# Performance work log

Hardware: AMD Instinct MI355X
Metric: run time of the kernel (lower is better)

Reference implementation:

```python
import jax, jax.numpy as jnp
import numpy as np

V, E, HD, K = 100000, 128, 256, 9
B, T = 128, 512
H = HD // 2  # per-direction hidden size


def setup_inputs() -> dict:
    key = jax.random.key(0)
    ks = jax.random.split(key, 16)
    s = 0.1
    rn = lambda k, shape: jax.random.normal(k, shape, jnp.float32) * s
    sentences = jax.random.randint(ks[0], (B, T), 0, V, dtype=jnp.int32)
    lengths = jax.random.randint(ks[1], (B,), 1, T + 1, dtype=jnp.int32)
    return {
        'sentences': sentences,
        'lengths': lengths,
        'embed': rn(ks[2], (V, E)),
        'Wih_f': rn(ks[3], (4 * H, E)), 'Whh_f': rn(ks[4], (4 * H, H)),
        'bih_f': rn(ks[5], (4 * H,)), 'bhh_f': rn(ks[6], (4 * H,)),
        'Wih_b': rn(ks[7], (4 * H, E)), 'Whh_b': rn(ks[8], (4 * H, H)),
        'bih_b': rn(ks[9], (4 * H,)), 'bhh_b': rn(ks[10], (4 * H,)),
        'W_out': rn(ks[11], (K, HD)), 'b_out': rn(ks[12], (K,)),
        'start_t': rn(ks[13], (K,)), 'end_t': rn(ks[14], (K,)),
        'trans': rn(ks[15], (K, K)),
    }


def _lstm(x, mask, Wih, Whh, bih, bhh, reverse):
    # x: [B,T,E], mask: [B,T] bool. Replicates packed-sequence semantics:
    # state frozen and output zeroed at padding positions (padding is trailing,
    # so reverse=True starts fresh at each sequence's true end).
    Bv, Hv = x.shape[0], Whh.shape[1]
    bias = bih + bhh

    def step(carry, inp):
        h, c = carry
        x_t, m_t = inp  # [B,E], [B,1]
        gates = x_t @ Wih.T + h @ Whh.T + bias  # [B,4H]
        i, f, g, o = jnp.split(gates, 4, axis=-1)  # torch gate order i,f,g,o
        c_new = jax.nn.sigmoid(f) * c + jax.nn.sigmoid(i) * jnp.tanh(g)
        h_new = jax.nn.sigmoid(o) * jnp.tanh(c_new)
        h = jnp.where(m_t, h_new, h)
        c = jnp.where(m_t, c_new, c)
        return (h, c), h * m_t.astype(h.dtype)

    init = (jnp.zeros((Bv, Hv), x.dtype), jnp.zeros((Bv, Hv), x.dtype))
    xs = (jnp.swapaxes(x, 0, 1), jnp.swapaxes(mask, 0, 1)[..., None])
    _, hs = jax.lax.scan(step, init, xs, reverse=reverse)
    return jnp.swapaxes(hs, 0, 1)  # [B,T,H]


def _emissions(sentences, mask, embed, Wih_f, Whh_f, bih_f, bhh_f,
               Wih_b, Whh_b, bih_b, bhh_b, W_out, b_out):
    x = embed[sentences]  # [B,T,E] (dropout is identity at inference)
    hf = _lstm(x, mask, Wih_f, Whh_f, bih_f, bhh_f, reverse=False)
    hb = _lstm(x, mask, Wih_b, Whh_b, bih_b, bhh_b, reverse=True)
    h = jnp.concatenate([hf, hb], axis=-1)  # [B,T,2H]
    return jnp.einsum('btd,kd->btk', h, W_out) + b_out  # [B,T,K]


def _viterbi(em, mask, start_t, end_t, trans):
    # torchcrf-style batched Viterbi decode. em: [B,T,K], mask: [B,T] bool.
    Kv = em.shape[-1]
    ident = jnp.arange(Kv, dtype=jnp.int32)[None]  # identity backpointers for pads
    score0 = start_t[None] + em[:, 0]  # [B,K]

    def step(score, inp):
        em_t, m_t = inp  # [B,K], [B,1]
        cand = score[:, :, None] + trans[None] + em_t[:, None, :]  # [B,K_prev,K_cur]
        new_score = cand.max(axis=1)
        idx = cand.argmax(axis=1).astype(jnp.int32)  # [B,K]
        score = jnp.where(m_t, new_score, score)
        idx = jnp.where(m_t, idx, ident)
        return score, idx

    xs = (jnp.swapaxes(em[:, 1:], 0, 1), jnp.swapaxes(mask[:, 1:], 0, 1)[..., None])
    score, hist = jax.lax.scan(step, score0, xs)  # hist: [T-1,B,K]
    score = score + end_t[None]
    last_tag = jnp.argmax(score, axis=-1).astype(jnp.int32)  # [B]

    def back(tag, idx_t):
        prev = jnp.take_along_axis(idx_t, tag[:, None], axis=1)[:, 0]
        return prev, prev

    _, tags_prev = jax.lax.scan(back, last_tag, hist, reverse=True)  # [T-1,B]
    tags = jnp.swapaxes(jnp.concatenate([tags_prev, last_tag[None]], axis=0), 0, 1)
    return jnp.where(mask, tags, 0), score.max(axis=-1)


def reference(sentences, lengths, embed, Wih_f, Whh_f, bih_f, bhh_f,
              Wih_b, Whh_b, bih_b, bhh_b, W_out, b_out, start_t, end_t, trans):
    mask = jnp.arange(sentences.shape[1])[None] < lengths[:, None]  # [B,T]
    em = _emissions(sentences, mask, embed, Wih_f, Whh_f, bih_f, bhh_f,
                    Wih_b, Whh_b, bih_b, bhh_b, W_out, b_out)
    tags, _ = _viterbi(em, mask, start_t, end_t, trans)
    return tags  # [B,T] int32, padded positions set to 0
```

## Files before the change

kernel.cpp:

```cpp
#include <hip/hip_runtime.h>
#include <cmath>

#define B_  128
#define T_  512
#define E_  128
#define H_  128
#define G4  512
#define K_  9

__global__ __launch_bounds__(256, 2)
void proj_gemm(const int* __restrict__ sent, const float* __restrict__ embed,
               const float* __restrict__ Wf, const float* __restrict__ Wb,
               const float* __restrict__ bif, const float* __restrict__ bhf,
               const float* __restrict__ bib, const float* __restrict__ bhb,
               float* __restrict__ proj, int t0f, int Tc)
{
  __shared__ __align__(16) float Al[128 * 64];
  __shared__ __align__(16) float Bl[128 * 64];
  const int tid   = threadIdx.x;
  const int ntile = blockIdx.x;
  const int mtile = blockIdx.y;
  const int tpb   = Tc >> 6;
  const int b     = mtile / tpb;
  const int toff  = (mtile - b * tpb) << 6;
  const int dir   = ntile >> 3;
  const int t0    = dir ? (T_ - t0f - Tc) : t0f;
  const float* __restrict__ W = dir ? Wb : Wf;
  const int n0 = (ntile & 7) << 6;

  {
    const int r  = tid & 63;
    const int kc = tid >> 6;
    const int t  = t0 + toff + r;
    const int vid = sent[b * T_ + t];
    const float* arow = embed + (size_t)vid * E_ + kc * 32;
    const float* brow = W + (size_t)(n0 + r) * E_ + kc * 32;
#pragma unroll
    for (int q = 0; q < 8; ++q) {
      float4 av = *(const float4*)(arow + q * 4);
      float4 bv = *(const float4*)(brow + q * 4);
      int k0 = kc * 32 + q * 4;
      Al[(k0 + 0) * 64 + r] = av.x; Al[(k0 + 1) * 64 + r] = av.y;
      Al[(k0 + 2) * 64 + r] = av.z; Al[(k0 + 3) * 64 + r] = av.w;
      Bl[(k0 + 0) * 64 + r] = bv.x; Bl[(k0 + 1) * 64 + r] = bv.y;
      Bl[(k0 + 2) * 64 + r] = bv.z; Bl[(k0 + 3) * 64 + r] = bv.w;
    }
  }
  __syncthreads();

  const int mg = tid & 15, ng = tid >> 4;
  float acc[4][4] = {};
#pragma unroll 8
  for (int k = 0; k < 128; ++k) {
    float4 a  = *(const float4*)&Al[k * 64 + mg * 4];
    float4 bb = *(const float4*)&Bl[k * 64 + ng * 4];
    acc[0][0] += a.x * bb.x; acc[0][1] += a.x * bb.y; acc[0][2] += a.x * bb.z; acc[0][3] += a.x * bb.w;
    acc[1][0] += a.y * bb.x; acc[1][1] += a.y * bb.y; acc[1][2] += a.y * bb.z; acc[1][3] += a.y * bb.w;
    acc[2][0] += a.z * bb.x; acc[2][1] += a.z * bb.y; acc[2][2] += a.z * bb.z; acc[2][3] += a.z * bb.w;
    acc[3][0] += a.w * bb.x; acc[3][1] += a.w * bb.y; acc[3][2] += a.w * bb.z; acc[3][3] += a.w * bb.w;
  }

  const float* bi = dir ? bib : bif;
  const float* bh = dir ? bhb : bhf;
  const int nl = ng * 4;
  float4 bias;
  bias.x = bi[n0 + nl + 0] + bh[n0 + nl + 0];
  bias.y = bi[n0 + nl + 1] + bh[n0 + nl + 1];
  bias.z = bi[n0 + nl + 2] + bh[n0 + nl + 2];
  bias.w = bi[n0 + nl + 3] + bh[n0 + nl + 3];
#pragma unroll
  for (int i = 0; i < 4; ++i) {
    const int tloc = toff + mg * 4 + i;
    float4 o;
    o.x = acc[i][0] + bias.x; o.y = acc[i][1] + bias.y;
    o.z = acc[i][2] + bias.z; o.w = acc[i][3] + bias.w;
    *(float4*)&proj[((size_t)(b * Tc + tloc)) * 1024 + dir * G4 + n0 + nl] = o;
  }
}

__global__ __launch_bounds__(512, 2)
void lstm_chunk(const float* __restrict__ proj,
                const float* __restrict__ Whf, const float* __restrict__ Whb,
                const int* __restrict__ lengths,
                float* __restrict__ hs,
                float* __restrict__ sh, float* __restrict__ sc,
                int t0f, int Tc, int first)
{
  const int dir = blockIdx.x;
  const int b   = blockIdx.y;
  const int tid = threadIdx.x;
  const float* __restrict__ Whh = dir ? Whb : Whf;
  __shared__ __align__(16) float h_lds[H_];
  __shared__ float gates[G4];

  float w[128];
  {
    const float* wr = Whh + (size_t)tid * H_;
#pragma unroll
    for (int k = 0; k < 128; k += 4) {
      float4 v = *(const float4*)(wr + k);
      w[k] = v.x; w[k + 1] = v.y; w[k + 2] = v.z; w[k + 3] = v.w;
    }
  }
  const int len = lengths[b];
  const int t0  = dir ? (T_ - t0f - Tc) : t0f;
  float c = 0.f;
  if (tid < H_) {
    if (first) {
      h_lds[tid] = 0.f;
    } else {
      h_lds[tid] = sh[(dir * B_ + b) * H_ + tid];
      c          = sc[(dir * B_ + b) * H_ + tid];
    }
  }
  __syncthreads();

  const float* projp = proj + (size_t)b * Tc * 1024 + dir * G4 + tid;
  for (int s = 0; s < Tc; ++s) {
    const int tc = dir ? (Tc - 1 - s) : s;
    const int t  = t0 + tc;
    float acc = projp[(size_t)tc * 1024];
#pragma unroll
    for (int k4 = 0; k4 < 32; ++k4) {
      float4 h4 = *(const float4*)&h_lds[k4 * 4];
      acc += w[4 * k4 + 0] * h4.x; acc += w[4 * k4 + 1] * h4.y;
      acc += w[4 * k4 + 2] * h4.z; acc += w[4 * k4 + 3] * h4.w;
    }
    const int blk = tid >> 7;
    gates[tid] = (blk == 2) ? tanhf(acc) : 1.f / (1.f + expf(-acc));
    __syncthreads();
    if (tid < H_) {
      float gi = gates[tid], gf = gates[tid + 128];
      float gg = gates[tid + 256], go = gates[tid + 384];
      float cn = gf * c + gi * gg;
      float hn = go * tanhf(cn);
      bool  m  = (t < len);
      float hold = h_lds[tid];
      c = m ? cn : c;
      h_lds[tid] = m ? hn : hold;
      hs[(size_t)(b * T_ + t) * 256 + dir * H_ + tid] = m ? hn : 0.f;
    }
    __syncthreads();
  }
  if (tid < H_) {
    sh[(dir * B_ + b) * H_ + tid] = h_lds[tid];
    sc[(dir * B_ + b) * H_ + tid] = c;
  }
}

__global__ __launch_bounds__(256)
void emis_kernel(const float* __restrict__ hs, const float* __restrict__ Wout,
                 const float* __restrict__ bout, float* __restrict__ em)
{
  __shared__ __align__(16) float Wl[K_ * 256];
  const int tid = threadIdx.x;
  for (int i = tid; i < K_ * 256; i += 256) Wl[i] = Wout[i];
  __syncthreads();
  const int m = blockIdx.x * 256 + tid;
  const float* h = hs + (size_t)m * 256;
  float acc[K_] = {};
#pragma unroll 4
  for (int kk = 0; kk < 64; ++kk) {
    float4 h4 = *(const float4*)(h + kk * 4);
#pragma unroll
    for (int k9 = 0; k9 < K_; ++k9) {
      float4 w4 = *(const float4*)&Wl[k9 * 256 + kk * 4];
      acc[k9] += h4.x * w4.x + h4.y * w4.y + h4.z * w4.z + h4.w * w4.w;
    }
  }
#pragma unroll
  for (int k9 = 0; k9 < K_; ++k9) em[(size_t)m * K_ + k9] = acc[k9] + bout[k9];
}

__global__ __launch_bounds__(64)
void viterbi_kernel(const float* __restrict__ em, const int* __restrict__ lengths,
                    const float* __restrict__ st, const float* __restrict__ en,
                    const float* __restrict__ trans, int* __restrict__ tags)
{
  const int b    = blockIdx.x;
  const int lane = threadIdx.x;
  __shared__ unsigned char hist[(T_ - 1) * 16];
  const int len = lengths[b];
  float tr[K_];
#pragma unroll
  for (int j = 0; j < K_; ++j) tr[j] = (lane < K_) ? trans[j * K_ + lane] : 0.f;
  float s = (lane < K_) ? st[lane] + em[(size_t)(b * T_) * K_ + lane] : -1e30f;
  for (int t = 1; t < len; ++t) {
    float best = -1e30f; int bj = 0;
#pragma unroll
    for (int j = 0; j < K_; ++j) {
      float v = __shfl(s, j) + tr[j];
      if (v > best) { best = v; bj = j; }
    }
    if (lane < K_) {
      s = best + em[(size_t)(b * T_ + t) * K_ + lane];
      hist[(t - 1) * 16 + lane] = (unsigned char)bj;
    }
  }
  float fs = (lane < K_) ? s + en[lane] : -1e30f;
  float best = -1e30f; int last = 0;
#pragma unroll
  for (int j = 0; j < K_; ++j) {
    float v = __shfl(fs, j);
    if (v > best) { best = v; last = j; }
  }
  __syncthreads();
  if (lane == 0) {
    int tag = last;
    tags[b * T_ + len - 1] = tag;
    for (int t = len - 2; t >= 0; --t) {
      tag = hist[t * 16 + tag];
      tags[b * T_ + t] = tag;
    }
  }
  for (int t = len + lane; t < T_; t += 64) tags[b * T_ + t] = 0;
}

extern "C" void kernel_launch(void* const* d_in, const int* in_sizes, int n_in,
                              void* d_out, int out_size, void* d_ws, size_t ws_size,
                              hipStream_t stream)
{
  const int*   sent  = (const int*)d_in[0];
  const int*   lens  = (const int*)d_in[1];
  const float* embed = (const float*)d_in[2];
  const float* Wif   = (const float*)d_in[3];
  const float* Whf   = (const float*)d_in[4];
  const float* bif   = (const float*)d_in[5];
  const float* bhf   = (const float*)d_in[6];
  const float* Wib   = (const float*)d_in[7];
  const float* Whb   = (const float*)d_in[8];
  const float* bib   = (const float*)d_in[9];
  const float* bhb   = (const float*)d_in[10];
  const float* Wout  = (const float*)d_in[11];
  const float* bout  = (const float*)d_in[12];
  const float* stt   = (const float*)d_in[13];
  const float* ent   = (const float*)d_in[14];
  const float* trans = (const float*)d_in[15];
  int* tags = (int*)d_out;

  float* ws   = (float*)d_ws;
  float* hs   = ws;
  float* em   = hs + (size_t)B_ * T_ * 256;
  float* sh   = em + (size_t)B_ * T_ * K_;
  float* sc   = sh + (size_t)2 * B_ * H_;
  float* proj = sc + (size_t)2 * B_ * H_;
  const size_t fixed_bytes = (size_t)(proj - ws) * sizeof(float);

  int Tc = 512;
  while (Tc > 64 && fixed_bytes + (size_t)B_ * Tc * 1024 * sizeof(float) > ws_size)
    Tc >>= 1;

  const int nch = T_ / Tc;
  for (int c2 = 0; c2 < nch; ++c2) {
    const int t0f = c2 * Tc;
    dim3 g1(16, B_ * (Tc >> 6));
    hipLaunchKernelGGL(proj_gemm, g1, dim3(256), 0, stream,
                       sent, embed, Wif, Wib, bif, bhf, bib, bhb, proj, t0f, Tc);
    dim3 g2(2, B_);
    hipLaunchKernelGGL(lstm_chunk, g2, dim3(512), 0, stream,
                       proj, Whf, Whb, lens, hs, sh, sc, t0f, Tc, (int)(c2 == 0));
  }
  hipLaunchKernelGGL(emis_kernel, dim3((B_ * T_) / 256), dim3(256), 0, stream,
                     hs, Wout, bout, em);
  hipLaunchKernelGGL(viterbi_kernel, dim3(B_), dim3(64), 0, stream,
                     em, lens, stt, ent, trans, tags);
}
```

Before: 1.043 ms.

## Replace LDS-tiled projection GEMM with register-resident weight row kernel

The input projection GEMM is rewritten so each lane holds one full 128-wide weight row in registers and streams embedding rows, which are wave-uniform via readfirstlane, computing two output rows per iteration. This removes the LDS staging and the per-tile reload of the weight matrix. In exchange it uses a large register footprint (128 floats per lane), which lowers occupancy, and embedding rows are re-read by every wave group instead of shared through LDS.

```diff
diff --git a/kernel.cpp b/kernel.cpp
--- a/kernel.cpp
+++ b/kernel.cpp
@@ -9,72 +9,71 @@
 #define K_  9
 
 __global__ __launch_bounds__(256, 2)
-void proj_gemm(const int* __restrict__ sent, const float* __restrict__ embed,
-               const float* __restrict__ Wf, const float* __restrict__ Wb,
-               const float* __restrict__ bif, const float* __restrict__ bhf,
-               const float* __restrict__ bib, const float* __restrict__ bhb,
-               float* __restrict__ proj, int t0f, int Tc)
-{
-  __shared__ __align__(16) float Al[128 * 64];
-  __shared__ __align__(16) float Bl[128 * 64];
-  const int tid   = threadIdx.x;
-  const int ntile = blockIdx.x;
-  const int mtile = blockIdx.y;
-  const int tpb   = Tc >> 6;
-  const int b     = mtile / tpb;
-  const int toff  = (mtile - b * tpb) << 6;
-  const int dir   = ntile >> 3;
-  const int t0    = dir ? (T_ - t0f - Tc) : t0f;
+void proj_gemm2(const int* __restrict__ sent, const float* __restrict__ embed,
+                const float* __restrict__ Wf, const float* __restrict__ Wb,
+                const float* __restrict__ bif, const float* __restrict__ bhf,
+                const float* __restrict__ bib, const float* __restrict__ bhb,
+                float* __restrict__ proj, int t0f, int Tc, int tcshift,
+                int rows_per_block)
+{
+  const int lane = threadIdx.x & 63;
+  const int wv   = __builtin_amdgcn_readfirstlane((int)(threadIdx.x >> 6));
+  const int ngrp = __builtin_amdgcn_readfirstlane((int)(blockIdx.x * 4 + wv));
+  const int dir  = ngrp >> 3;
+  const int nsub = (ngrp & 7) << 6;
+  const int nrow = nsub + lane;
   const float* __restrict__ W = dir ? Wb : Wf;
-  const int n0 = (ntile & 7) << 6;
-
-  {
-    const int r  = tid & 63;
-    const int kc = tid >> 6;
-    const int t  = t0 + toff + r;
-    const int vid = sent[b * T_ + t];
-    const float* arow = embed + (size_t)vid * E_ + kc * 32;
-    const float* brow = W + (size_t)(n0 + r) * E_ + kc * 32;
-#pragma unroll
-    for (int q = 0; q < 8; ++q) {
-      float4 av = *(const float4*)(arow + q * 4);
-      float4 bv = *(const float4*)(brow + q * 4);
-      int k0 = kc * 32 + q * 4;
-      Al[(k0 + 0) * 64 + r] = av.x; Al[(k0 + 1) * 64 + r] = av.y;
-      Al[(k0 + 2) * 64 + r] = av.z; Al[(k0 + 3) * 64 + r] = av.w;
-      Bl[(k0 + 0) * 64 + r] = bv.x; Bl[(k0 + 1) * 64 + r] = bv.y;
-      Bl[(k0 + 2) * 64 + r] = bv.z; Bl[(k0 + 3) * 64 + r] = bv.w;
-    }
-  }
-  __syncthreads();
-
-  const int mg = tid & 15, ng = tid >> 4;
-  float acc[4][4] = {};
-#pragma unroll 8
-  for (int k = 0; k < 128; ++k) {
-    float4 a  = *(const float4*)&Al[k * 64 + mg * 4];
-    float4 bb = *(const float4*)&Bl[k * 64 + ng * 4];
-    acc[0][0] += a.x * bb.x; acc[0][1] += a.x * bb.y; acc[0][2] += a.x * bb.z; acc[0][3] += a.x * bb.w;
-    acc[1][0] += a.y * bb.x; acc[1][1] += a.y * bb.y; acc[1][2] += a.y * bb.z; acc[1][3] += a.y * bb.w;
-    acc[2][0] += a.z * bb.x; acc[2][1] += a.z * bb.y; acc[2][2] += a.z * bb.z; acc[2][3] += a.z * bb.w;
-    acc[3][0] += a.w * bb.x; acc[3][1] += a.w * bb.y; acc[3][2] += a.w * bb.z; acc[3][3] += a.w * bb.w;
-  }
-
   const float* bi = dir ? bib : bif;
   const float* bh = dir ? bhb : bhf;
-  const int nl = ng * 4;
-  float4 bias;
-  bias.x = bi[n0 + nl + 0] + bh[n0 + nl + 0];
-  bias.y = bi[n0 + nl + 1] + bh[n0 + nl + 1];
-  bias.z = bi[n0 + nl + 2] + bh[n0 + nl + 2];
-  bias.w = bi[n0 + nl + 3] + bh[n0 + nl + 3];
-#pragma unroll
-  for (int i = 0; i < 4; ++i) {
-    const int tloc = toff + mg * 4 + i;
-    float4 o;
-    o.x = acc[i][0] + bias.x; o.y = acc[i][1] + bias.y;
-    o.z = acc[i][2] + bias.z; o.w = acc[i][3] + bias.w;
-    *(float4*)&proj[((size_t)(b * Tc + tloc)) * 1024 + dir * G4 + n0 + nl] = o;
+
+  float w[128];
+#pragma unroll
+  for (int k = 0; k < 128; k += 4) {
+    float4 v = *(const float4*)(W + (size_t)nrow * E_ + k);
+    w[k] = v.x; w[k + 1] = v.y; w[k + 2] = v.z; w[k + 3] = v.w;
+  }
+  const float bias = bi[nrow] + bh[nrow];
+
+  const int t0  = dir ? (T_ - t0f - Tc) : t0f;
+  const int tcm = Tc - 1;
+  const int r0  = blockIdx.y * rows_per_block;
+
+  for (int r = r0; r < r0 + rows_per_block; r += 2) {
+    const int ba = r >> tcshift,        bb2 = (r + 1) >> tcshift;
+    const int ta = t0 + (r & tcm),      tb  = t0 + ((r + 1) & tcm);
+    const int va = __builtin_amdgcn_readfirstlane(sent[ba * T_ + ta]);
+    const int vb = __builtin_amdgcn_readfirstlane(sent[bb2 * T_ + tb]);
+    const float4* ea = (const float4*)(embed + (size_t)va * E_);
+    const float4* eb = (const float4*)(embed + (size_t)vb * E_);
+
+    float pa0 = 0.f, pa1 = 0.f, pa2 = 0.f, pa3 = 0.f;
+    float pb0 = 0.f, pb1 = 0.f, pb2 = 0.f, pb3 = 0.f;
+#pragma unroll
+    for (int q = 0; q < 32; q += 4) {
+      float4 xa0 = ea[q + 0], xa1 = ea[q + 1], xa2 = ea[q + 2], xa3 = ea[q + 3];
+      float4 xb0 = eb[q + 0], xb1 = eb[q + 1], xb2 = eb[q + 2], xb3 = eb[q + 3];
+      const int k = 4 * q;
+      pa0 += w[k + 0] * xa0.x;  pa0 += w[k + 1] * xa0.y;
+      pa0 += w[k + 2] * xa0.z;  pa0 += w[k + 3] * xa0.w;
+      pb0 += w[k + 0] * xb0.x;  pb0 += w[k + 1] * xb0.y;
+      pb0 += w[k + 2] * xb0.z;  pb0 += w[k + 3] * xb0.w;
+      pa1 += w[k + 4] * xa1.x;  pa1 += w[k + 5] * xa1.y;
+      pa1 += w[k + 6] * xa1.z;  pa1 += w[k + 7] * xa1.w;
+      pb1 += w[k + 4] * xb1.x;  pb1 += w[k + 5] * xb1.y;
+      pb1 += w[k + 6] * xb1.z;  pb1 += w[k + 7] * xb1.w;
+      pa2 += w[k + 8] * xa2.x;  pa2 += w[k + 9] * xa2.y;
+      pa2 += w[k +10] * xa2.z;  pa2 += w[k +11] * xa2.w;
+      pb2 += w[k + 8] * xb2.x;  pb2 += w[k + 9] * xb2.y;
+      pb2 += w[k +10] * xb2.z;  pb2 += w[k +11] * xb2.w;
+      pa3 += w[k +12] * xa3.x;  pa3 += w[k +13] * xa3.y;
+      pa3 += w[k +14] * xa3.z;  pa3 += w[k +15] * xa3.w;
+      pb3 += w[k +12] * xb3.x;  pb3 += w[k +13] * xb3.y;
+      pb3 += w[k +14] * xb3.z;  pb3 += w[k +15] * xb3.w;
+    }
+    const float sa = ((pa0 + pa1) + (pa2 + pa3)) + bias;
+    const float sb = ((pb0 + pb1) + (pb2 + pb3)) + bias;
+    proj[(size_t)r       * 1024 + dir * G4 + nsub + lane] = sa;
+    proj[(size_t)(r + 1) * 1024 + dir * G4 + nsub + lane] = sb;
   }
 }
 
@@ -246,16 +245,20 @@
   float* proj = sc + (size_t)2 * B_ * H_;
   const size_t fixed_bytes = (size_t)(proj - ws) * sizeof(float);
 
-  int Tc = 512;
-  while (Tc > 64 && fixed_bytes + (size_t)B_ * Tc * 1024 * sizeof(float) > ws_size)
-    Tc >>= 1;
+  int Tc = 512, tcshift = 9;
+  while (Tc > 64 && fixed_bytes + (size_t)B_ * Tc * 1024 * sizeof(float) > ws_size) {
+    Tc >>= 1; tcshift--;
+  }
 
   const int nch = T_ / Tc;
   for (int c2 = 0; c2 < nch; ++c2) {
     const int t0f = c2 * Tc;
-    dim3 g1(16, B_ * (Tc >> 6));
-    hipLaunchKernelGGL(proj_gemm, g1, dim3(256), 0, stream,
-                       sent, embed, Wif, Wib, bif, bhf, bib, bhb, proj, t0f, Tc);
+    const int rows = B_ * Tc;
+    const int rpb  = rows / 256;
+    dim3 g1(4, 256);
+    hipLaunchKernelGGL(proj_gemm2, g1, dim3(256), 0, stream,
+                       sent, embed, Wif, Wib, bif, bhf, bib, bhb,
+                       proj, t0f, Tc, tcshift, rpb);
     dim3 g2(2, B_);
     hipLaunchKernelGGL(lstm_chunk, g2, dim3(512), 0, stream,
                        proj, Whf, Whb, lens, hs, sh, sc, t0f, Tc, (int)(c2 == 0));
```

After: 1.420 ms. 1.36x slower.
